# Kernel optimization log

Hardware: AMD Instinct MI355X
Metric: run time of the kernel (lower is better)

Reference implementation:

```python
import jax, jax.numpy as jnp
import numpy as np

B, S, E, U = 4, 512, 512, 256

def setup_inputs() -> dict:
    key = jax.random.key(0)
    k1, k2, k3, k4 = jax.random.split(key, 4)
    h1 = jax.random.normal(k1, (B, S, E), dtype=jnp.float32)
    h2 = jax.random.normal(k2, (B, S, E), dtype=jnp.float32)
    # glorot-ish scaled weights
    w = jax.random.normal(k3, (2 * E, U), dtype=jnp.float32) * (2.0 / (2 * E + U)) ** 0.5
    b1 = jnp.zeros((U,), dtype=jnp.float32)
    v = jax.random.normal(k4, (U, 1), dtype=jnp.float32) * (2.0 / (U + 1)) ** 0.5
    b2 = jnp.zeros((1,), dtype=jnp.float32)
    return {"h1": h1, "h2": h2, "w": w, "b1": b1, "v": v, "b2": b2}

def reference(h1, h2, w, b1, v, b2):
    # Original: for each query step i, concat([h1, repeat(h2[:,i])]) @ w.
    # Split w so the concat-matmul becomes two separate projections:
    #   concat([h1_j, h2_i]) @ w == h1_j @ w1 + h2_i @ w2
    E_ = h1.shape[-1]
    w1, w2 = w[:E_], w[E_:]
    key_pre = jnp.einsum('bje,eu->bju', h1, w1)   # [B,Sk,U]
    qry_pre = jnp.einsum('bie,eu->biu', h2, w2)   # [B,Sq,U]
    # energy: [B,Sq,Sk,U]
    t = jnp.tanh(qry_pre[:, :, None, :] + key_pre[:, None, :, :] + b1)
    scores = jnp.einsum('biju,uo->bij', t, v) + b2[0]  # [B,Sq,Sk]
    p = jax.nn.softmax(scores, axis=-1)                # softmax over keys j
    # context per query: sum_j p[b,i,j] * h1[b,j]
    return jnp.einsum('bij,bje->bie', p, h1)           # [B,S,E]
```

## Files before the change

### kernel.cpp

```cpp
#include <hip/hip_runtime.h>
#include <hip/hip_bf16.h>

#define B_ 4
#define S_ 512
#define E_ 512
#define U_ 256

#define KC 2.885390081777927f

#if __has_builtin(__builtin_amdgcn_exp2f)
#define EXP2F(x) __builtin_amdgcn_exp2f(x)
#else
#define EXP2F(x) __exp2f(x)
#endif
#if __has_builtin(__builtin_amdgcn_rcpf)
#define RCPF(x) __builtin_amdgcn_rcpf(x)
#else
#define RCPF(x) (1.0f / (x))
#endif

typedef __attribute__((ext_vector_type(8))) short bf16x8;
typedef __attribute__((ext_vector_type(4))) float f32x4;

__device__ __forceinline__ unsigned short bf16rn(float x) {
    unsigned int u = __float_as_uint(x);
    u = (u + 0x7FFFu + ((u >> 16) & 1u)) >> 16;
    return (unsigned short)u;
}
__device__ __forceinline__ void splitT(float x, short* hi, short* lo) {
    const unsigned u = __float_as_uint(x);
    *hi = (short)(u >> 16);
    const float hf = __uint_as_float(u & 0xFFFF0000u);
    *lo = (short)(__float_as_uint(x - hf) >> 16);
}

__global__ __launch_bounds__(256) void prep_gemm(
    const float* __restrict__ h1, const float* __restrict__ h2,
    const float* __restrict__ w, const float* __restrict__ b1,
    float* __restrict__ keySt, float* __restrict__ qryS,
    bf16x8* __restrict__ h1c)
{
    __shared__ unsigned short WhiL[2][16][64][8];
    __shared__ unsigned short WloL[2][16][64][8];

    const int tid = threadIdx.x;
    const int bid = blockIdx.x;

    if (bid < 512) {
        const int z = bid >> 8, ngg = (bid >> 5) & 7, mq = bid & 31;

        const int r8 = tid >> 5, ul = tid & 31;
        const int ntc = ul >> 4, l16c = ul & 15;
        const float* __restrict__ Wp = w + (size_t)z * E_ * U_ + ngg * 32 + ul;
#pragma unroll 4
        for (int it = 0; it < 64; ++it) {
            const int k = it * 8 + r8;
            short h, l;
            splitT(Wp[(size_t)k * U_] * KC, &h, &l);
            const int kc = k >> 5, quad = (k >> 3) & 3, jj = k & 7;
            WhiL[ntc][kc][quad * 16 + l16c][jj] = (unsigned short)h;
            WloL[ntc][kc][quad * 16 + l16c][jj] = (unsigned short)l;
        }
        __syncthreads();

        const int wv = tid >> 6, lane = tid & 63;
        const int quad = lane >> 4, l16 = lane & 15;
        const int m0 = (mq * 4 + wv) * 16;
        const float* __restrict__ Arow = (z ? h2 : h1) + (size_t)(m0 + l16) * E_;

        f32x4 acc[2];
        acc[0] = (f32x4){0.f, 0.f, 0.f, 0.f};
        acc[1] = (f32x4){0.f, 0.f, 0.f, 0.f};

        for (int kc = 0; kc < 16; ++kc) {
            const int kb = kc * 32 + quad * 8;
            const float4 x0 = *(const float4*)&Arow[kb];
            const float4 x1 = *(const float4*)&Arow[kb + 4];
            const float xs[8] = {x0.x, x0.y, x0.z, x0.w, x1.x, x1.y, x1.z, x1.w};
            bf16x8 ah, al;
#pragma unroll
            for (int j = 0; j < 8; ++j) {
                short h, l; splitT(xs[j], &h, &l);
                ah[j] = h; al[j] = l;
            }
#pragma unroll
            for (int nt = 0; nt < 2; ++nt) {
                const bf16x8 bh = *(const bf16x8*)&WhiL[nt][kc][lane][0];
                const bf16x8 bl = *(const bf16x8*)&WloL[nt][kc][lane][0];
                acc[nt] = __builtin_amdgcn_mfma_f32_16x16x32_bf16(ah, bh, acc[nt], 0, 0, 0);
                acc[nt] = __builtin_amdgcn_mfma_f32_16x16x32_bf16(ah, bl, acc[nt], 0, 0, 0);
                acc[nt] = __builtin_amdgcn_mfma_f32_16x16x32_bf16(al, bh, acc[nt], 0, 0, 0);
            }
        }

        if (z == 0) {
            const int b = m0 >> 9;
            const int j0 = (m0 & (S_ - 1)) + quad * 4;
#pragma unroll
            for (int nt = 0; nt < 2; ++nt) {
                const int u = (ngg * 2 + nt) * 16 + l16;
                *(float4*)&keySt[((size_t)b * U_ + u) * S_ + j0] =
                    make_float4(acc[nt][0], acc[nt][1], acc[nt][2], acc[nt][3]);
            }
        } else {
            const int row = m0 + quad * 4;
#pragma unroll
            for (int nt = 0; nt < 2; ++nt) {
                const int u = (ngg * 2 + nt) * 16 + l16;
                const float bias = KC * b1[u];
#pragma unroll
                for (int r = 0; r < 4; ++r)
                    qryS[(size_t)(row + r) * U_ + u] = acc[nt][r] + bias;
            }
        }
    } else {
        const int s = (bid - 512) * 256 + tid;
        const int lane = s & 63, kc = (s >> 6) & 15, et = (s >> 10) & 31, b = s >> 15;
        const int quad = lane >> 4, l16 = lane & 15;
        const float* __restrict__ src =
            h1 + ((size_t)b * S_ + kc * 32 + quad * 8) * E_ + et * 16 + l16;
        bf16x8 c;
#pragma unroll
        for (int j = 0; j < 8; ++j)
            c[j] = (short)bf16rn(src[(size_t)j * E_]);
        h1c[s] = c;
    }
}

__device__ __forceinline__ float quadTerm(float a0, float a1, float a2, float a3,
                                          float4 vq, float acc) {
    const float F1 = EXP2F(a0) + 1.f;
    const float F2 = EXP2F(a1) + 1.f;
    const float F3 = EXP2F(a2) + 1.f;
    const float F4 = EXP2F(a3) + 1.f;
    const float P12 = F1 * F2, P34 = F3 * F4;
    const float n12 = fmaf(vq.y, F1, vq.x * F2);
    const float n34 = fmaf(vq.w, F3, vq.z * F4);
    const float num = fmaf(n34, P12, n12 * P34);
    return fmaf(num, RCPF(P12 * P34), acc);
}

__global__ __launch_bounds__(512) void scores_kernel(
    const float* __restrict__ keySt, const float* __restrict__ qryS,
    const float* __restrict__ v, unsigned short* __restrict__ Pp)
{
    const int i0 = blockIdx.x * 4;
    const int b = blockIdx.y;
    const int t = threadIdx.x;
    const int wv = t >> 6;

    __shared__ float ssm[8][4];

    const float4* __restrict__ q0v = (const float4*)(qryS + ((size_t)b * S_ + i0) * U_);
    const float4* __restrict__ q1v = q0v + (U_ / 4);
    const float4* __restrict__ q2v = q0v + 2 * (U_ / 4);
    const float4* __restrict__ q3v = q0v + 3 * (U_ / 4);
    const float4* __restrict__ vv4 = (const float4*)v;
    const float* __restrict__ kb = keySt + (size_t)b * U_ * S_ + t;

    float a0 = 0.f, a1 = 0.f, a2 = 0.f, a3 = 0.f;
#pragma unroll 4
    for (int ub = 0; ub < U_ / 4; ++ub) {
        const float4 vq = vv4[ub];
        const float k0 = kb[(size_t)(ub * 4 + 0) * S_];
        const float k1 = kb[(size_t)(ub * 4 + 1) * S_];
        const float k2 = kb[(size_t)(ub * 4 + 2) * S_];
        const float k3 = kb[(size_t)(ub * 4 + 3) * S_];
        const float4 q0 = q0v[ub], q1 = q1v[ub], q2 = q2v[ub], q3 = q3v[ub];
        a0 = quadTerm(q0.x + k0, q0.y + k1, q0.z + k2, q0.w + k3, vq, a0);
        a1 = quadTerm(q1.x + k0, q1.y + k1, q1.z + k2, q1.w + k3, vq, a1);
        a2 = quadTerm(q2.x + k0, q2.y + k1, q2.z + k2, q2.w + k3, vq, a2);
        a3 = quadTerm(q3.x + k0, q3.y + k1, q3.z + k2, q3.w + k3, vq, a3);
    }

    const float p0 = EXP2F(-a0 * KC);
    const float p1 = EXP2F(-a1 * KC);
    const float p2 = EXP2F(-a2 * KC);
    const float p3 = EXP2F(-a3 * KC);
    float s0 = p0, s1 = p1, s2 = p2, s3 = p3;
#pragma unroll
    for (int off = 1; off < 64; off <<= 1) {
        s0 += __shfl_xor(s0, off, 64);
        s1 += __shfl_xor(s1, off, 64);
        s2 += __shfl_xor(s2, off, 64);
        s3 += __shfl_xor(s3, off, 64);
    }
    if ((t & 63) == 0) {
        ssm[wv][0] = s0; ssm[wv][1] = s1; ssm[wv][2] = s2; ssm[wv][3] = s3;
    }
    __syncthreads();
    s0 = ssm[0][0]; s1 = ssm[0][1]; s2 = ssm[0][2]; s3 = ssm[0][3];
#pragma unroll
    for (int k = 1; k < 8; ++k) {
        s0 += ssm[k][0]; s1 += ssm[k][1]; s2 += ssm[k][2]; s3 += ssm[k][3];
    }
    const float r0 = RCPF(s0), r1 = RCPF(s1), r2 = RCPF(s2), r3 = RCPF(s3);

    const int itile = i0 >> 4;
    const int base = (itile * 16 + (t >> 5)) * 64 + (((t >> 3) & 3) << 4);
    unsigned short* __restrict__ pb = Pp + (size_t)b * S_ * S_;
    const int io = i0 & 15, jo = t & 7;
    pb[((base + io + 0) << 3) + jo] = bf16rn(p0 * r0);
    pb[((base + io + 1) << 3) + jo] = bf16rn(p1 * r1);
    pb[((base + io + 2) << 3) + jo] = bf16rn(p2 * r2);
    pb[((base + io + 3) << 3) + jo] = bf16rn(p3 * r3);
}

__global__ __launch_bounds__(256) void pv_gemm(
    const unsigned short* __restrict__ Pp, const bf16x8* __restrict__ h1c,
    float* __restrict__ out)
{
    const int tid = threadIdx.x;
    const int wv = tid >> 6, lane = tid & 63;
    const int quad = lane >> 4, l16 = lane & 15;
    const int wt = blockIdx.x * 4 + wv;
    const int b = wt >> 8, rem = wt & 255;
    const int it = rem >> 3, eg = rem & 7;

    const bf16x8* __restrict__ Ab =
        (const bf16x8*)(Pp + (size_t)b * S_ * S_) + (it * 16) * 64 + lane;
    const bf16x8* __restrict__ Bb =
        h1c + ((b * 32 + eg * 4) * 16) * 64 + lane;

    f32x4 acc[4];
#pragma unroll
    for (int i = 0; i < 4; ++i) acc[i] = (f32x4){0.f, 0.f, 0.f, 0.f};

    for (int kc = 0; kc < 16; ++kc) {
        const bf16x8 a8 = Ab[kc * 64];
#pragma unroll
        for (int n = 0; n < 4; ++n) {
            const bf16x8 b8 = Bb[(n * 16 + kc) * 64];
            acc[n] = __builtin_amdgcn_mfma_f32_16x16x32_bf16(a8, b8, acc[n], 0, 0, 0);
        }
    }

    const int i = it * 16 + quad * 4;
#pragma unroll
    for (int n = 0; n < 4; ++n) {
        const int e = (eg * 4 + n) * 16 + l16;
        float* __restrict__ ob = out + ((size_t)b * S_ + i) * E_ + e;
#pragma unroll
        for (int r = 0; r < 4; ++r)
            ob[(size_t)r * E_] = acc[n][r];
    }
}

extern "C" void kernel_launch(void* const* d_in, const int* in_sizes, int n_in,
                              void* d_out, int out_size, void* d_ws, size_t ws_size,
                              hipStream_t stream) {
    const float* h1 = (const float*)d_in[0];
    const float* h2 = (const float*)d_in[1];
    const float* w  = (const float*)d_in[2];
    const float* b1 = (const float*)d_in[3];
    const float* v  = (const float*)d_in[4];
    float* out = (float*)d_out;

    char* ws = (char*)d_ws;
    float* keySt = (float*)ws;                 ws += 2u << 20;
    float* qryS  = (float*)ws;                 ws += 2u << 20;
    unsigned short* Pp = (unsigned short*)ws;  ws += 2u << 20;
    bf16x8* h1c = (bf16x8*)ws;

    prep_gemm<<<dim3(1024), dim3(256), 0, stream>>>(h1, h2, w, b1, keySt, qryS, h1c);
    scores_kernel<<<dim3(S_ / 4, B_), dim3(512), 0, stream>>>(keySt, qryS, v, Pp);
    pv_gemm<<<dim3(256), dim3(256), 0, stream>>>(Pp, h1c, out);
}
```

Measured before the change: 136.8 us.

## Factor tanh exponent as product of precomputed exponentials; move h1 conversion into scores kernel

Precomputes exp2 of the scaled key and query projections in the GEMM epilogue, so the O(B·S²·U) scores loop computes each tanh denominator term as fmaf(eq, ek, 1) and no longer evaluates an exponential per element. The h1-to-bf16 packing moves from the prep kernel into extra blocks of the scores kernel, and pv_gemm uses narrower per-wave tiles with twice as many blocks. The factorised exponentials can overflow or underflow when projections are large, which changes accuracy behaviour.

```diff
diff --git a/kernel.cpp b/kernel.cpp
--- a/kernel.cpp
+++ b/kernel.cpp
@@ -37,8 +37,7 @@
 __global__ __launch_bounds__(256) void prep_gemm(
     const float* __restrict__ h1, const float* __restrict__ h2,
     const float* __restrict__ w, const float* __restrict__ b1,
-    float* __restrict__ keySt, float* __restrict__ qryS,
-    bf16x8* __restrict__ h1c)
+    float* __restrict__ ekS, float* __restrict__ eqS)
 {
     __shared__ unsigned short WhiL[2][16][64][8];
     __shared__ unsigned short WloL[2][16][64][8];
@@ -46,75 +45,95 @@
     const int tid = threadIdx.x;
     const int bid = blockIdx.x;
 
-    if (bid < 512) {
-        const int z = bid >> 8, ngg = (bid >> 5) & 7, mq = bid & 31;
-
-        const int r8 = tid >> 5, ul = tid & 31;
-        const int ntc = ul >> 4, l16c = ul & 15;
-        const float* __restrict__ Wp = w + (size_t)z * E_ * U_ + ngg * 32 + ul;
+    const int z = bid >> 8, ngg = (bid >> 5) & 7, mq = bid & 31;
+
+    const int r8 = tid >> 5, ul = tid & 31;
+    const int ntc = ul >> 4, l16c = ul & 15;
+    const float* __restrict__ Wp = w + (size_t)z * E_ * U_ + ngg * 32 + ul;
 #pragma unroll 4
-        for (int it = 0; it < 64; ++it) {
-            const int k = it * 8 + r8;
-            short h, l;
-            splitT(Wp[(size_t)k * U_] * KC, &h, &l);
-            const int kc = k >> 5, quad = (k >> 3) & 3, jj = k & 7;
-            WhiL[ntc][kc][quad * 16 + l16c][jj] = (unsigned short)h;
-            WloL[ntc][kc][quad * 16 + l16c][jj] = (unsigned short)l;
-        }
-        __syncthreads();
-
-        const int wv = tid >> 6, lane = tid & 63;
-        const int quad = lane >> 4, l16 = lane & 15;
-        const int m0 = (mq * 4 + wv) * 16;
-        const float* __restrict__ Arow = (z ? h2 : h1) + (size_t)(m0 + l16) * E_;
-
-        f32x4 acc[2];
-        acc[0] = (f32x4){0.f, 0.f, 0.f, 0.f};
-        acc[1] = (f32x4){0.f, 0.f, 0.f, 0.f};
-
-        for (int kc = 0; kc < 16; ++kc) {
-            const int kb = kc * 32 + quad * 8;
-            const float4 x0 = *(const float4*)&Arow[kb];
-            const float4 x1 = *(const float4*)&Arow[kb + 4];
-            const float xs[8] = {x0.x, x0.y, x0.z, x0.w, x1.x, x1.y, x1.z, x1.w};
-            bf16x8 ah, al;
-#pragma unroll
-            for (int j = 0; j < 8; ++j) {
-                short h, l; splitT(xs[j], &h, &l);
-                ah[j] = h; al[j] = l;
-            }
-#pragma unroll
-            for (int nt = 0; nt < 2; ++nt) {
-                const bf16x8 bh = *(const bf16x8*)&WhiL[nt][kc][lane][0];
-                const bf16x8 bl = *(const bf16x8*)&WloL[nt][kc][lane][0];
-                acc[nt] = __builtin_amdgcn_mfma_f32_16x16x32_bf16(ah, bh, acc[nt], 0, 0, 0);
-                acc[nt] = __builtin_amdgcn_mfma_f32_16x16x32_bf16(ah, bl, acc[nt], 0, 0, 0);
-                acc[nt] = __builtin_amdgcn_mfma_f32_16x16x32_bf16(al, bh, acc[nt], 0, 0, 0);
-            }
-        }
-
-        if (z == 0) {
-            const int b = m0 >> 9;
-            const int j0 = (m0 & (S_ - 1)) + quad * 4;
-#pragma unroll
-            for (int nt = 0; nt < 2; ++nt) {
-                const int u = (ngg * 2 + nt) * 16 + l16;
-                *(float4*)&keySt[((size_t)b * U_ + u) * S_ + j0] =
-                    make_float4(acc[nt][0], acc[nt][1], acc[nt][2], acc[nt][3]);
-            }
-        } else {
-            const int row = m0 + quad * 4;
-#pragma unroll
-            for (int nt = 0; nt < 2; ++nt) {
-                const int u = (ngg * 2 + nt) * 16 + l16;
-                const float bias = KC * b1[u];
-#pragma unroll
-                for (int r = 0; r < 4; ++r)
-                    qryS[(size_t)(row + r) * U_ + u] = acc[nt][r] + bias;
-            }
+    for (int it = 0; it < 64; ++it) {
+        const int k = it * 8 + r8;
+        short h, l;
+        splitT(Wp[(size_t)k * U_] * KC, &h, &l);
+        const int kc = k >> 5, quad = (k >> 3) & 3, jj = k & 7;
+        WhiL[ntc][kc][quad * 16 + l16c][jj] = (unsigned short)h;
+        WloL[ntc][kc][quad * 16 + l16c][jj] = (unsigned short)l;
+    }
+    __syncthreads();
+
+    const int wv = tid >> 6, lane = tid & 63;
+    const int quad = lane >> 4, l16 = lane & 15;
+    const int m0 = (mq * 4 + wv) * 16;
+    const float* __restrict__ Arow = (z ? h2 : h1) + (size_t)(m0 + l16) * E_;
+
+    f32x4 acc[2];
+    acc[0] = (f32x4){0.f, 0.f, 0.f, 0.f};
+    acc[1] = (f32x4){0.f, 0.f, 0.f, 0.f};
+
+    for (int kc = 0; kc < 16; ++kc) {
+        const int kb = kc * 32 + quad * 8;
+        const float4 x0 = *(const float4*)&Arow[kb];
+        const float4 x1 = *(const float4*)&Arow[kb + 4];
+        const float xs[8] = {x0.x, x0.y, x0.z, x0.w, x1.x, x1.y, x1.z, x1.w};
+        bf16x8 ah, al;
+#pragma unroll
+        for (int j = 0; j < 8; ++j) {
+            short h, l; splitT(xs[j], &h, &l);
+            ah[j] = h; al[j] = l;
+        }
+#pragma unroll
+        for (int nt = 0; nt < 2; ++nt) {
+            const bf16x8 bh = *(const bf16x8*)&WhiL[nt][kc][lane][0];
+            const bf16x8 bl = *(const bf16x8*)&WloL[nt][kc][lane][0];
+            acc[nt] = __builtin_amdgcn_mfma_f32_16x16x32_bf16(ah, bh, acc[nt], 0, 0, 0);
+            acc[nt] = __builtin_amdgcn_mfma_f32_16x16x32_bf16(ah, bl, acc[nt], 0, 0, 0);
+            acc[nt] = __builtin_amdgcn_mfma_f32_16x16x32_bf16(al, bh, acc[nt], 0, 0, 0);
+        }
+    }
+
+    if (z == 0) {
+        const int b = m0 >> 9;
+        const int j0 = (m0 & (S_ - 1)) + quad * 4;
+#pragma unroll
+        for (int nt = 0; nt < 2; ++nt) {
+            const int u = (ngg * 2 + nt) * 16 + l16;
+            *(float4*)&ekS[((size_t)b * U_ + u) * S_ + j0] =
+                make_float4(EXP2F(acc[nt][0]), EXP2F(acc[nt][1]),
+                            EXP2F(acc[nt][2]), EXP2F(acc[nt][3]));
         }
     } else {
-        const int s = (bid - 512) * 256 + tid;
+        const int row = m0 + quad * 4;
+#pragma unroll
+        for (int nt = 0; nt < 2; ++nt) {
+            const int u = (ngg * 2 + nt) * 16 + l16;
+            const float bias = KC * b1[u];
+#pragma unroll
+            for (int r = 0; r < 4; ++r)
+                eqS[(size_t)(row + r) * U_ + u] = EXP2F(acc[nt][r] + bias);
+        }
+    }
+}
+
+__device__ __forceinline__ float quadG(float G1, float G2, float G3, float G4,
+                                       float4 vq, float acc) {
+    const float P12 = G1 * G2, P34 = G3 * G4;
+    const float n12 = fmaf(vq.y, G1, vq.x * G2);
+    const float n34 = fmaf(vq.w, G3, vq.z * G4);
+    const float num = fmaf(n34, P12, n12 * P34);
+    return fmaf(num, RCPF(P12 * P34), acc);
+}
+
+__global__ __launch_bounds__(512) void scores_kernel(
+    const float* __restrict__ ekS, const float* __restrict__ eqS,
+    const float* __restrict__ v, unsigned short* __restrict__ Pp,
+    const float* __restrict__ h1, bf16x8* __restrict__ h1c)
+{
+    __shared__ float ssm[8][4];
+    const int bid = blockIdx.x;
+    const int t = threadIdx.x;
+
+    if (bid >= 512) {
+        const int s = (bid - 512) * 512 + t;
         const int lane = s & 63, kc = (s >> 6) & 15, et = (s >> 10) & 31, b = s >> 15;
         const int quad = lane >> 4, l16 = lane & 15;
         const float* __restrict__ src =
@@ -124,53 +143,37 @@
         for (int j = 0; j < 8; ++j)
             c[j] = (short)bf16rn(src[(size_t)j * E_]);
         h1c[s] = c;
-    }
-}
-
-__device__ __forceinline__ float quadTerm(float a0, float a1, float a2, float a3,
-                                          float4 vq, float acc) {
-    const float F1 = EXP2F(a0) + 1.f;
-    const float F2 = EXP2F(a1) + 1.f;
-    const float F3 = EXP2F(a2) + 1.f;
-    const float F4 = EXP2F(a3) + 1.f;
-    const float P12 = F1 * F2, P34 = F3 * F4;
-    const float n12 = fmaf(vq.y, F1, vq.x * F2);
-    const float n34 = fmaf(vq.w, F3, vq.z * F4);
-    const float num = fmaf(n34, P12, n12 * P34);
-    return fmaf(num, RCPF(P12 * P34), acc);
-}
-
-__global__ __launch_bounds__(512) void scores_kernel(
-    const float* __restrict__ keySt, const float* __restrict__ qryS,
-    const float* __restrict__ v, unsigned short* __restrict__ Pp)
-{
-    const int i0 = blockIdx.x * 4;
-    const int b = blockIdx.y;
-    const int t = threadIdx.x;
+        return;
+    }
+
+    const int b = bid & 3;
+    const int i0 = (bid >> 2) * 4;
     const int wv = t >> 6;
 
-    __shared__ float ssm[8][4];
-
-    const float4* __restrict__ q0v = (const float4*)(qryS + ((size_t)b * S_ + i0) * U_);
+    const float4* __restrict__ q0v = (const float4*)(eqS + ((size_t)b * S_ + i0) * U_);
     const float4* __restrict__ q1v = q0v + (U_ / 4);
     const float4* __restrict__ q2v = q0v + 2 * (U_ / 4);
     const float4* __restrict__ q3v = q0v + 3 * (U_ / 4);
     const float4* __restrict__ vv4 = (const float4*)v;
-    const float* __restrict__ kb = keySt + (size_t)b * U_ * S_ + t;
+    const float* __restrict__ kb = ekS + (size_t)b * U_ * S_ + t;
 
     float a0 = 0.f, a1 = 0.f, a2 = 0.f, a3 = 0.f;
 #pragma unroll 4
     for (int ub = 0; ub < U_ / 4; ++ub) {
         const float4 vq = vv4[ub];
-        const float k0 = kb[(size_t)(ub * 4 + 0) * S_];
-        const float k1 = kb[(size_t)(ub * 4 + 1) * S_];
-        const float k2 = kb[(size_t)(ub * 4 + 2) * S_];
-        const float k3 = kb[(size_t)(ub * 4 + 3) * S_];
+        const float e0 = kb[(size_t)(ub * 4 + 0) * S_];
+        const float e1 = kb[(size_t)(ub * 4 + 1) * S_];
+        const float e2 = kb[(size_t)(ub * 4 + 2) * S_];
+        const float e3 = kb[(size_t)(ub * 4 + 3) * S_];
         const float4 q0 = q0v[ub], q1 = q1v[ub], q2 = q2v[ub], q3 = q3v[ub];
-        a0 = quadTerm(q0.x + k0, q0.y + k1, q0.z + k2, q0.w + k3, vq, a0);
-        a1 = quadTerm(q1.x + k0, q1.y + k1, q1.z + k2, q1.w + k3, vq, a1);
-        a2 = quadTerm(q2.x + k0, q2.y + k1, q2.z + k2, q2.w + k3, vq, a2);
-        a3 = quadTerm(q3.x + k0, q3.y + k1, q3.z + k2, q3.w + k3, vq, a3);
+        a0 = quadG(fmaf(q0.x, e0, 1.f), fmaf(q0.y, e1, 1.f),
+                   fmaf(q0.z, e2, 1.f), fmaf(q0.w, e3, 1.f), vq, a0);
+        a1 = quadG(fmaf(q1.x, e0, 1.f), fmaf(q1.y, e1, 1.f),
+                   fmaf(q1.z, e2, 1.f), fmaf(q1.w, e3, 1.f), vq, a1);
+        a2 = quadG(fmaf(q2.x, e0, 1.f), fmaf(q2.y, e1, 1.f),
+                   fmaf(q2.z, e2, 1.f), fmaf(q2.w, e3, 1.f), vq, a2);
+        a3 = quadG(fmaf(q3.x, e0, 1.f), fmaf(q3.y, e1, 1.f),
+                   fmaf(q3.z, e2, 1.f), fmaf(q3.w, e3, 1.f), vq, a3);
     }
 
     const float p0 = EXP2F(-a0 * KC);
@@ -214,22 +217,22 @@
     const int wv = tid >> 6, lane = tid & 63;
     const int quad = lane >> 4, l16 = lane & 15;
     const int wt = blockIdx.x * 4 + wv;
-    const int b = wt >> 8, rem = wt & 255;
-    const int it = rem >> 3, eg = rem & 7;
+    const int b = wt >> 9, rem = wt & 511;
+    const int it = rem >> 4, eg = rem & 15;
 
     const bf16x8* __restrict__ Ab =
         (const bf16x8*)(Pp + (size_t)b * S_ * S_) + (it * 16) * 64 + lane;
     const bf16x8* __restrict__ Bb =
-        h1c + ((b * 32 + eg * 4) * 16) * 64 + lane;
-
-    f32x4 acc[4];
-#pragma unroll
-    for (int i = 0; i < 4; ++i) acc[i] = (f32x4){0.f, 0.f, 0.f, 0.f};
+        h1c + ((b * 32 + eg * 2) * 16) * 64 + lane;
+
+    f32x4 acc[2];
+    acc[0] = (f32x4){0.f, 0.f, 0.f, 0.f};
+    acc[1] = (f32x4){0.f, 0.f, 0.f, 0.f};
 
     for (int kc = 0; kc < 16; ++kc) {
         const bf16x8 a8 = Ab[kc * 64];
 #pragma unroll
-        for (int n = 0; n < 4; ++n) {
+        for (int n = 0; n < 2; ++n) {
             const bf16x8 b8 = Bb[(n * 16 + kc) * 64];
             acc[n] = __builtin_amdgcn_mfma_f32_16x16x32_bf16(a8, b8, acc[n], 0, 0, 0);
         }
@@ -237,8 +240,8 @@
 
     const int i = it * 16 + quad * 4;
 #pragma unroll
-    for (int n = 0; n < 4; ++n) {
-        const int e = (eg * 4 + n) * 16 + l16;
+    for (int n = 0; n < 2; ++n) {
+        const int e = (eg * 2 + n) * 16 + l16;
         float* __restrict__ ob = out + ((size_t)b * S_ + i) * E_ + e;
 #pragma unroll
         for (int r = 0; r < 4; ++r)
@@ -257,12 +260,12 @@
     float* out = (float*)d_out;
 
     char* ws = (char*)d_ws;
-    float* keySt = (float*)ws;                 ws += 2u << 20;
-    float* qryS  = (float*)ws;                 ws += 2u << 20;
+    float* ekS = (float*)ws;                   ws += 2u << 20;
+    float* eqS = (float*)ws;                   ws += 2u << 20;
     unsigned short* Pp = (unsigned short*)ws;  ws += 2u << 20;
     bf16x8* h1c = (bf16x8*)ws;
 
-    prep_gemm<<<dim3(1024), dim3(256), 0, stream>>>(h1, h2, w, b1, keySt, qryS, h1c);
-    scores_kernel<<<dim3(S_ / 4, B_), dim3(512), 0, stream>>>(keySt, qryS, v, Pp);
-    pv_gemm<<<dim3(256), dim3(256), 0, stream>>>(Pp, h1c, out);
-}
+    prep_gemm<<<dim3(512), dim3(256), 0, stream>>>(h1, h2, w, b1, ekS, eqS);
+    scores_kernel<<<dim3(768), dim3(512), 0, stream>>>(ekS, eqS, v, Pp, h1, h1c);
+    pv_gemm<<<dim3(512), dim3(256), 0, stream>>>(Pp, h1c, out);
+}
```

After: 115.4 us. -15.6%, faster.
